# Performance work log

Hardware: AMD Instinct MI355X
Metric: run time of the kernel (lower is better)

## Reference

```python
import jax, jax.numpy as jnp
import numpy as np

NEG_INF = -1000000000.0
INPUT_SIZE = 1024
HIDDEN_SIZE = 64
B, S = 8, 2048


def setup_inputs() -> dict:
    key = jax.random.key(0)
    ks = jax.random.split(key, 8)
    scale = 1.0 / np.sqrt(INPUT_SIZE)
    inp = {
        "input": jax.random.normal(ks[0], (B, S, INPUT_SIZE), dtype=jnp.float32),
        "mask": jax.random.randint(ks[1], (B, S, S), 0, 2, dtype=jnp.int32),
        "W_q": jax.random.uniform(ks[2], (HIDDEN_SIZE, INPUT_SIZE), jnp.float32, -scale, scale),
        "b_q": jax.random.uniform(ks[3], (HIDDEN_SIZE,), jnp.float32, -scale, scale),
        "W_k": jax.random.uniform(ks[4], (HIDDEN_SIZE, INPUT_SIZE), jnp.float32, -scale, scale),
        "b_k": jax.random.uniform(ks[5], (HIDDEN_SIZE,), jnp.float32, -scale, scale),
        "W_v": jax.random.uniform(ks[6], (HIDDEN_SIZE, INPUT_SIZE), jnp.float32, -scale, scale),
        "b_v": jax.random.uniform(ks[7], (HIDDEN_SIZE,), jnp.float32, -scale, scale),
    }
    return inp


def reference(input, mask, W_q, b_q, W_k, b_k, W_v, b_v):
    inv_sqrt_d = 1.0 / np.sqrt(HIDDEN_SIZE)
    # Q/K/V projections: torch Linear is x @ W.T + b
    q = jnp.einsum('bsi,hi->bsh', input, W_q) + b_q  # (B,S,H)
    k = jnp.einsum('bsi,hi->bsh', input, W_k) + b_k
    v = jnp.einsum('bsi,hi->bsh', input, W_v) + b_v
    scores = jnp.einsum('bqh,bkh->bqk', q, k) * inv_sqrt_d  # (B,S,S)
    scores = jnp.where(mask == 0, NEG_INF, scores)
    probs = jax.nn.softmax(scores, axis=-1)
    return jnp.einsum('bqk,bkh->bqh', probs, v)  # (B,S,H)
```

## Files before the change

kernel.cpp:

```cpp
#include <hip/hip_runtime.h>

typedef __bf16 bf16;
typedef bf16 bf16x4 __attribute__((ext_vector_type(4)));
typedef bf16 bf16x8 __attribute__((ext_vector_type(8)));
typedef float floatx4 __attribute__((ext_vector_type(4)));
typedef unsigned int u32;

#define B_ 8
#define S_ 2048
#define I_ 1024
#define H_ 64

__device__ __forceinline__ void async_cp16(bf16* lds_base, const bf16* g_base, int lane) {
    __builtin_amdgcn_global_load_lds(
        (const __attribute__((address_space(1))) u32*)(g_base + lane * 8),
        (__attribute__((address_space(3))) u32*)lds_base, 16, 0, 0);
}

__global__ __launch_bounds__(256) void prep(const int* __restrict__ mask,
                                            u32* __restrict__ pm,
                                            const float* __restrict__ Wq, const float* __restrict__ bq,
                                            const float* __restrict__ Wk, const float* __restrict__ bk,
                                            const float* __restrict__ Wv, const float* __restrict__ bv,
                                            bf16* __restrict__ Wc2, float* __restrict__ bc) {
    if (blockIdx.x < 4096) {
        int d = blockIdx.x * 256 + threadIdx.x;
        const int4* src = (const int4*)(mask + (size_t)d * 32);
        u32 bits = 0;
#pragma unroll
        for (int j = 0; j < 8; ++j) {
            int4 v = src[j];
            bits |= (v.x != 0 ? 1u : 0u) << (j * 4);
            bits |= (v.y != 0 ? 1u : 0u) << (j * 4 + 1);
            bits |= (v.z != 0 ? 1u : 0u) << (j * 4 + 2);
            bits |= (v.w != 0 ? 1u : 0u) << (j * 4 + 3);
        }
        pm[d] = bits;
    } else {
        int idx = (blockIdx.x - 4096) * 256 + threadIdx.x;
        int n = idx >> 10, i = idx & 1023;
        float v;
        if (n < 64)       v = Wq[n * I_ + i] * 0.125f;
        else if (n < 128) v = Wk[(n - 64) * I_ + i];
        else              v = Wv[(n - 128) * I_ + i];
        int s = i >> 7, kl = i & 127;
        Wc2[(size_t)s * 26112 + n * 136 + kl] = (bf16)v;
        if (idx < 192) {
            float bb = (idx < 64) ? bq[idx] * 0.125f
                     : (idx < 128) ? bk[idx - 64] : bv[idx - 128];
            bc[idx] = bb;
        }
    }
}

__global__ __launch_bounds__(256, 2) void qkv_gemm(const float* __restrict__ X,
                                                   const bf16* __restrict__ Wc2,
                                                   const float* __restrict__ bc,
                                                   bf16* __restrict__ Qd,
                                                   bf16* __restrict__ Kd2,
                                                   bf16* __restrict__ Vt2) {
    __shared__ __align__(16) bf16 Xs[32 * 136];
    __shared__ __align__(16) bf16 Ws[26112];

    int tid = threadIdx.x;
    int w = tid >> 6, lane = tid & 63;
    int n = lane & 15, g = lane >> 4;
    int m0 = blockIdx.x * 32;
    int mt = w & 1, nh = (w >> 1) * 96;

    floatx4 zero4 = {0.0f, 0.0f, 0.0f, 0.0f};
    floatx4 acc[6];
#pragma unroll
    for (int t = 0; t < 6; ++t) acc[t] = zero4;

    int xrow = tid >> 3, xcb = (tid & 7) * 16;
    const float* xsrc = X + (size_t)(m0 + xrow) * I_ + xcb;
    bf16* xdst = Xs + xrow * 136 + xcb;

    float4 xr0 = *(const float4*)(xsrc);
    float4 xr1 = *(const float4*)(xsrc + 4);
    float4 xr2 = *(const float4*)(xsrc + 8);
    float4 xr3 = *(const float4*)(xsrc + 12);

    for (int s = 0; s < 8; ++s) {
#pragma unroll
        for (int i = 0; i < 13; ++i) {
            int inst = i * 4 + w;
            if (inst < 51)
                async_cp16(Ws + inst * 512, Wc2 + (size_t)s * 26112 + inst * 512, lane);
        }
        bf16x8 b0, b1;
        b0[0] = (bf16)xr0.x; b0[1] = (bf16)xr0.y; b0[2] = (bf16)xr0.z; b0[3] = (bf16)xr0.w;
        b0[4] = (bf16)xr1.x; b0[5] = (bf16)xr1.y; b0[6] = (bf16)xr1.z; b0[7] = (bf16)xr1.w;
        b1[0] = (bf16)xr2.x; b1[1] = (bf16)xr2.y; b1[2] = (bf16)xr2.z; b1[3] = (bf16)xr2.w;
        b1[4] = (bf16)xr3.x; b1[5] = (bf16)xr3.y; b1[6] = (bf16)xr3.z; b1[7] = (bf16)xr3.w;
        *(bf16x8*)xdst = b0;
        *(bf16x8*)(xdst + 8) = b1;
        __syncthreads();

        if (s < 7) {
            const float* xp = xsrc + (s + 1) * 128;
            xr0 = *(const float4*)(xp);
            xr1 = *(const float4*)(xp + 4);
            xr2 = *(const float4*)(xp + 8);
            xr3 = *(const float4*)(xp + 12);
        }

#pragma unroll
        for (int ks = 0; ks < 4; ++ks) {
            bf16x8 xa = *(bf16x8*)(Xs + (mt * 16 + n) * 136 + ks * 32 + g * 8);
#pragma unroll
            for (int nt = 0; nt < 6; ++nt) {
                bf16x8 wb = *(bf16x8*)(Ws + (nh + nt * 16 + n) * 136 + ks * 32 + g * 8);
                acc[nt] = __builtin_amdgcn_mfma_f32_16x16x32_bf16(xa, wb, acc[nt], 0, 0, 0);
            }
        }
        __syncthreads();
    }

    int b = m0 >> 11;
    int sb = (m0 & 2047) + mt * 16 + g * 4;
#pragma unroll
    for (int nt = 0; nt < 6; ++nt) {
        int ng = nh + nt * 16 + n;
        float bias = bc[ng];
        if (ng < 64) {
#pragma unroll
            for (int r = 0; r < 4; ++r)
                Qd[(size_t)(b * S_ + sb + r) * H_ + ng] = (bf16)(acc[nt][r] + bias);
        } else if (ng < 128) {
            int hc = (ng - 64) >> 3, j = (ng - 64) & 7;
#pragma unroll
            for (int r = 0; r < 4; ++r)
                Kd2[((size_t)(b * 8 + hc) * S_ + sb + r) * 8 + j] = (bf16)(acc[nt][r] + bias);
        } else {
            int hh = ng - 128, kc = sb >> 3, jj = sb & 7;
            bf16x4 pk;
#pragma unroll
            for (int r = 0; r < 4; ++r) pk[r] = (bf16)(acc[nt][r] + bias);
            *(bf16x4*)(Vt2 + ((size_t)(b * 256 + kc) * 64 + hh) * 8 + jj) = pk;
        }
    }
}

__global__ __launch_bounds__(256, 4) void attn(const bf16* __restrict__ Qd,
                                               const bf16* __restrict__ Kd2,
                                               const bf16* __restrict__ Vt2,
                                               const u32* __restrict__ pm,
                                               float* __restrict__ po,
                                               float* __restrict__ pl) {
    __shared__ __align__(16) bf16 regA[8704];
    __shared__ __align__(16) bf16 Vs[16 * 528];

    int tid = threadIdx.x;
    int w = tid >> 6, lane = tid & 63;
    int n = lane & 15, g = lane >> 4;
    int bid = blockIdx.x;
    int ksp = bid & 3;
    int qt = (bid >> 2) & 31;
    int b = bid >> 7;
    int q0 = qt * 64;

    const bf16* qptr = Qd + (size_t)(b * S_ + q0 + w * 16 + n) * H_ + g * 8;
    bf16x8 qa0 = *(const bf16x8*)qptr;
    bf16x8 qa1 = *(const bf16x8*)(qptr + 32);

    floatx4 zero4 = {0.0f, 0.0f, 0.0f, 0.0f};
    floatx4 o[4];
#pragma unroll
    for (int t = 0; t < 4; ++t) o[t] = zero4;
    float l_i[4] = {0.0f, 0.0f, 0.0f, 0.0f};

    const u32* pmb = pm + (size_t)(b * S_ + q0 + w * 16 + g * 4) * 64;

    for (int kt = ksp * 4; kt < ksp * 4 + 4; ++kt) {
        u32 mq[4][4];
#pragma unroll
        for (int r = 0; r < 4; ++r) {
            uint4 t4 = *(const uint4*)(pmb + (size_t)r * 64 + kt * 4);
            mq[r][0] = t4.x; mq[r][1] = t4.y; mq[r][2] = t4.z; mq[r][3] = t4.w;
        }
#pragma unroll
        for (int j = 0; j < 4; ++j) {
            int hc = w * 2 + (j >> 1), p = j & 1;
            async_cp16(regA + hc * 1040 + p * 512,
                       Kd2 + ((size_t)(b * 8 + hc) * S_ + kt * 128 + p * 64) * 8, lane);
        }
#pragma unroll
        for (int j = 0; j < 4; ++j) {
            int kcl = w * 4 + j;
            async_cp16(Vs + kcl * 528,
                       Vt2 + ((size_t)(b * 256 + kt * 16 + kcl) * 64) * 8, lane);
        }
        __syncthreads();

        floatx4 s[8];
#pragma unroll
        for (int nt = 0; nt < 8; ++nt) {
            floatx4 a = zero4;
            a = __builtin_amdgcn_mfma_f32_16x16x32_bf16(
                    qa0, *(const bf16x8*)(regA + g * 1040 + (nt * 16 + n) * 8), a, 0, 0, 0);
            a = __builtin_amdgcn_mfma_f32_16x16x32_bf16(
                    qa1, *(const bf16x8*)(regA + (4 + g) * 1040 + (nt * 16 + n) * 8), a, 0, 0, 0);
            s[nt] = a;
        }

#pragma unroll
        for (int r = 0; r < 4; ++r)
#pragma unroll
            for (int nt = 0; nt < 8; ++nt) {
                float e = __expf(s[nt][r]);
                bool bit = (mq[r][nt >> 1] >> ((nt & 1) * 16 + n)) & 1u;
                float p = bit ? e : 0.0f;
                s[nt][r] = p;
                l_i[r] += p;
            }
        __syncthreads();

#pragma unroll
        for (int r = 0; r < 4; ++r)
#pragma unroll
            for (int nt = 0; nt < 8; ++nt)
                regA[(w * 16 + g * 4 + r) * 136 + nt * 16 + n] = (bf16)s[nt][r];
        __syncthreads();

#pragma unroll
        for (int k0 = 0; k0 < 4; ++k0) {
            bf16x8 pa = *(bf16x8*)(regA + (w * 16 + n) * 136 + k0 * 32 + g * 8);
#pragma unroll
            for (int ht = 0; ht < 4; ++ht) {
                bf16x8 vb = *(bf16x8*)(Vs + (k0 * 4 + g) * 528 + (ht * 16 + n) * 8);
                o[ht] = __builtin_amdgcn_mfma_f32_16x16x32_bf16(pa, vb, o[ht], 0, 0, 0);
            }
        }
        __syncthreads();
    }

#pragma unroll
    for (int r = 0; r < 4; ++r)
#pragma unroll
        for (int off = 1; off < 16; off <<= 1)
            l_i[r] += __shfl_xor(l_i[r], off, 64);

    float* pb = po + (size_t)bid * 4096;
#pragma unroll
    for (int ht = 0; ht < 4; ++ht)
#pragma unroll
        for (int r = 0; r < 4; ++r)
            pb[(w * 16 + g * 4 + r) * 64 + ht * 16 + n] = o[ht][r];
    if (n == 0) {
#pragma unroll
        for (int r = 0; r < 4; ++r)
            pl[(size_t)bid * 64 + w * 16 + g * 4 + r] = l_i[r];
    }
}

__global__ __launch_bounds__(256) void reduce_o(const float* __restrict__ po,
                                                const float* __restrict__ pl,
                                                float* __restrict__ out) {
    int idx = blockIdx.x * 256 + threadIdx.x;
    int h = idx & 63, q = idx >> 6;
    int b = q >> 11, qq = q & 2047;
    int qt = qq >> 6, ql = qq & 63;
    int bid0 = (b * 32 + qt) * 4;
    float num = 0.0f, den = 0.0f;
#pragma unroll
    for (int j = 0; j < 4; ++j) {
        den += pl[(size_t)(bid0 + j) * 64 + ql];
        num += po[(size_t)(bid0 + j) * 4096 + ql * 64 + h];
    }
    out[(size_t)q * 64 + h] = num / den;
}

extern "C" void kernel_launch(void* const* d_in, const int* in_sizes, int n_in,
                              void* d_out, int out_size, void* d_ws, size_t ws_size,
                              hipStream_t stream) {
    const float* X    = (const float*)d_in[0];
    const int*   mask = (const int*)d_in[1];
    const float* Wq   = (const float*)d_in[2];
    const float* bq   = (const float*)d_in[3];
    const float* Wk   = (const float*)d_in[4];
    const float* bk   = (const float*)d_in[5];
    const float* Wv   = (const float*)d_in[6];
    const float* bv   = (const float*)d_in[7];
    float* out = (float*)d_out;

    char* p = (char*)d_ws;
    bf16* Qd   = (bf16*)p;  p += (size_t)B_ * S_ * H_ * 2;
    bf16* Kd2  = (bf16*)p;  p += (size_t)B_ * S_ * H_ * 2;
    bf16* Vt2  = (bf16*)p;  p += (size_t)B_ * S_ * H_ * 2;
    bf16* Wc2  = (bf16*)p;  p += (size_t)8 * 26112 * 2;
    float* bc  = (float*)p; p += 1024;
    u32*  pmb  = (u32*)p;   p += (size_t)B_ * S_ * 64 * 4;
    float* po  = (float*)p; p += (size_t)1024 * 4096 * 4;
    float* pl  = (float*)p; p += (size_t)1024 * 64 * 4;

    prep<<<dim3(4864), dim3(256), 0, stream>>>(mask, pmb, Wq, bq, Wk, bk, Wv, bv, Wc2, bc);
    qkv_gemm<<<dim3(512), dim3(256), 0, stream>>>(X, Wc2, bc, Qd, Kd2, Vt2);
    attn<<<dim3(1024), dim3(256), 0, stream>>>(Qd, Kd2, Vt2, pmb, po, pl);
    reduce_o<<<dim3(4096), dim3(256), 0, stream>>>(po, pl, out);
}
```

Measured before the change: 300.0 us.

## Fuse mask bit-packing into attention kernel via wave ballot

Removes the separate mask-packing pass and the packed-mask workspace. The attention kernel now reads the int32 mask directly, packs each row into bits with wave ballots into LDS, and reads the bitmask words from there. This drops one full write and read of the packed mask plus a kernel launch, but adds ballots and LDS traffic inside the attention loop. The QKV GEMM also stops prefetching the next X slice and loads it at the top of each step instead.

```diff
diff --git a/kernel.cpp b/kernel.cpp
--- a/kernel.cpp
+++ b/kernel.cpp
@@ -5,6 +5,7 @@
 typedef bf16 bf16x8 __attribute__((ext_vector_type(8)));
 typedef float floatx4 __attribute__((ext_vector_type(4)));
 typedef unsigned int u32;
+typedef unsigned long long u64;
 
 #define B_ 8
 #define S_ 2048
@@ -17,39 +18,22 @@
         (__attribute__((address_space(3))) u32*)lds_base, 16, 0, 0);
 }
 
-__global__ __launch_bounds__(256) void prep(const int* __restrict__ mask,
-                                            u32* __restrict__ pm,
-                                            const float* __restrict__ Wq, const float* __restrict__ bq,
-                                            const float* __restrict__ Wk, const float* __restrict__ bk,
-                                            const float* __restrict__ Wv, const float* __restrict__ bv,
-                                            bf16* __restrict__ Wc2, float* __restrict__ bc) {
-    if (blockIdx.x < 4096) {
-        int d = blockIdx.x * 256 + threadIdx.x;
-        const int4* src = (const int4*)(mask + (size_t)d * 32);
-        u32 bits = 0;
-#pragma unroll
-        for (int j = 0; j < 8; ++j) {
-            int4 v = src[j];
-            bits |= (v.x != 0 ? 1u : 0u) << (j * 4);
-            bits |= (v.y != 0 ? 1u : 0u) << (j * 4 + 1);
-            bits |= (v.z != 0 ? 1u : 0u) << (j * 4 + 2);
-            bits |= (v.w != 0 ? 1u : 0u) << (j * 4 + 3);
-        }
-        pm[d] = bits;
-    } else {
-        int idx = (blockIdx.x - 4096) * 256 + threadIdx.x;
-        int n = idx >> 10, i = idx & 1023;
-        float v;
-        if (n < 64)       v = Wq[n * I_ + i] * 0.125f;
-        else if (n < 128) v = Wk[(n - 64) * I_ + i];
-        else              v = Wv[(n - 128) * I_ + i];
-        int s = i >> 7, kl = i & 127;
-        Wc2[(size_t)s * 26112 + n * 136 + kl] = (bf16)v;
-        if (idx < 192) {
-            float bb = (idx < 64) ? bq[idx] * 0.125f
-                     : (idx < 128) ? bk[idx - 64] : bv[idx - 128];
-            bc[idx] = bb;
-        }
+__global__ void conv_w(const float* __restrict__ Wq, const float* __restrict__ bq,
+                       const float* __restrict__ Wk, const float* __restrict__ bk,
+                       const float* __restrict__ Wv, const float* __restrict__ bv,
+                       bf16* __restrict__ Wc2, float* __restrict__ bc) {
+    int idx = blockIdx.x * 256 + threadIdx.x;
+    int n = idx >> 10, i = idx & 1023;
+    float v;
+    if (n < 64)       v = Wq[n * I_ + i] * 0.125f;
+    else if (n < 128) v = Wk[(n - 64) * I_ + i];
+    else              v = Wv[(n - 128) * I_ + i];
+    int s = i >> 7, kl = i & 127;
+    Wc2[(size_t)s * 26112 + n * 136 + kl] = (bf16)v;
+    if (idx < 192) {
+        float bb = (idx < 64) ? bq[idx] * 0.125f
+                 : (idx < 128) ? bk[idx - 64] : bv[idx - 128];
+        bc[idx] = bb;
     }
 }
 
@@ -77,12 +61,12 @@
     const float* xsrc = X + (size_t)(m0 + xrow) * I_ + xcb;
     bf16* xdst = Xs + xrow * 136 + xcb;
 
-    float4 xr0 = *(const float4*)(xsrc);
-    float4 xr1 = *(const float4*)(xsrc + 4);
-    float4 xr2 = *(const float4*)(xsrc + 8);
-    float4 xr3 = *(const float4*)(xsrc + 12);
-
     for (int s = 0; s < 8; ++s) {
+        const float* xp = xsrc + s * 128;
+        float4 x0 = *(const float4*)(xp);
+        float4 x1 = *(const float4*)(xp + 4);
+        float4 x2 = *(const float4*)(xp + 8);
+        float4 x3 = *(const float4*)(xp + 12);
 #pragma unroll
         for (int i = 0; i < 13; ++i) {
             int inst = i * 4 + w;
@@ -90,21 +74,13 @@
                 async_cp16(Ws + inst * 512, Wc2 + (size_t)s * 26112 + inst * 512, lane);
         }
         bf16x8 b0, b1;
-        b0[0] = (bf16)xr0.x; b0[1] = (bf16)xr0.y; b0[2] = (bf16)xr0.z; b0[3] = (bf16)xr0.w;
-        b0[4] = (bf16)xr1.x; b0[5] = (bf16)xr1.y; b0[6] = (bf16)xr1.z; b0[7] = (bf16)xr1.w;
-        b1[0] = (bf16)xr2.x; b1[1] = (bf16)xr2.y; b1[2] = (bf16)xr2.z; b1[3] = (bf16)xr2.w;
-        b1[4] = (bf16)xr3.x; b1[5] = (bf16)xr3.y; b1[6] = (bf16)xr3.z; b1[7] = (bf16)xr3.w;
+        b0[0] = (bf16)x0.x; b0[1] = (bf16)x0.y; b0[2] = (bf16)x0.z; b0[3] = (bf16)x0.w;
+        b0[4] = (bf16)x1.x; b0[5] = (bf16)x1.y; b0[6] = (bf16)x1.z; b0[7] = (bf16)x1.w;
+        b1[0] = (bf16)x2.x; b1[1] = (bf16)x2.y; b1[2] = (bf16)x2.z; b1[3] = (bf16)x2.w;
+        b1[4] = (bf16)x3.x; b1[5] = (bf16)x3.y; b1[6] = (bf16)x3.z; b1[7] = (bf16)x3.w;
         *(bf16x8*)xdst = b0;
         *(bf16x8*)(xdst + 8) = b1;
         __syncthreads();
-
-        if (s < 7) {
-            const float* xp = xsrc + (s + 1) * 128;
-            xr0 = *(const float4*)(xp);
-            xr1 = *(const float4*)(xp + 4);
-            xr2 = *(const float4*)(xp + 8);
-            xr3 = *(const float4*)(xp + 12);
-        }
 
 #pragma unroll
         for (int ks = 0; ks < 4; ++ks) {
@@ -146,11 +122,12 @@
 __global__ __launch_bounds__(256, 4) void attn(const bf16* __restrict__ Qd,
                                                const bf16* __restrict__ Kd2,
                                                const bf16* __restrict__ Vt2,
-                                               const u32* __restrict__ pm,
+                                               const int* __restrict__ mask,
                                                float* __restrict__ po,
                                                float* __restrict__ pl) {
     __shared__ __align__(16) bf16 regA[8704];
     __shared__ __align__(16) bf16 Vs[16 * 528];
+    __shared__ __align__(16) u32 bfm[64][4];
 
     int tid = threadIdx.x;
     int w = tid >> 6, lane = tid & 63;
@@ -171,15 +148,15 @@
     for (int t = 0; t < 4; ++t) o[t] = zero4;
     float l_i[4] = {0.0f, 0.0f, 0.0f, 0.0f};
 
-    const u32* pmb = pm + (size_t)(b * S_ + q0 + w * 16 + g * 4) * 64;
+    const int* msl = mask + (size_t)(b * S_ + q0 + w * 16) * S_ + lane;
 
     for (int kt = ksp * 4; kt < ksp * 4 + 4; ++kt) {
-        u32 mq[4][4];
-#pragma unroll
-        for (int r = 0; r < 4; ++r) {
-            uint4 t4 = *(const uint4*)(pmb + (size_t)r * 64 + kt * 4);
-            mq[r][0] = t4.x; mq[r][1] = t4.y; mq[r][2] = t4.z; mq[r][3] = t4.w;
-        }
+        int mv[16][2];
+#pragma unroll
+        for (int rr = 0; rr < 16; ++rr)
+#pragma unroll
+            for (int c = 0; c < 2; ++c)
+                mv[rr][c] = msl[(size_t)rr * S_ + kt * 128 + c * 64];
 #pragma unroll
         for (int j = 0; j < 4; ++j) {
             int hc = w * 2 + (j >> 1), p = j & 1;
@@ -192,7 +169,24 @@
             async_cp16(Vs + kcl * 528,
                        Vt2 + ((size_t)(b * 256 + kt * 16 + kcl) * 64) * 8, lane);
         }
-        __syncthreads();
+#pragma unroll
+        for (int rr = 0; rr < 16; ++rr)
+#pragma unroll
+            for (int c = 0; c < 2; ++c) {
+                u64 bits = __ballot(mv[rr][c] != 0);
+                if (lane == 0) {
+                    bfm[w * 16 + rr][c * 2]     = (u32)bits;
+                    bfm[w * 16 + rr][c * 2 + 1] = (u32)(bits >> 32);
+                }
+            }
+        __syncthreads();
+
+        u32 mq[4][4];
+#pragma unroll
+        for (int r = 0; r < 4; ++r) {
+            uint4 t4 = *(const uint4*)&bfm[w * 16 + g * 4 + r][0];
+            mq[r][0] = t4.x; mq[r][1] = t4.y; mq[r][2] = t4.z; mq[r][3] = t4.w;
+        }
 
         floatx4 s[8];
 #pragma unroll
@@ -291,12 +285,11 @@
     bf16* Vt2  = (bf16*)p;  p += (size_t)B_ * S_ * H_ * 2;
     bf16* Wc2  = (bf16*)p;  p += (size_t)8 * 26112 * 2;
     float* bc  = (float*)p; p += 1024;
-    u32*  pmb  = (u32*)p;   p += (size_t)B_ * S_ * 64 * 4;
     float* po  = (float*)p; p += (size_t)1024 * 4096 * 4;
     float* pl  = (float*)p; p += (size_t)1024 * 64 * 4;
 
-    prep<<<dim3(4864), dim3(256), 0, stream>>>(mask, pmb, Wq, bq, Wk, bk, Wv, bv, Wc2, bc);
+    conv_w<<<dim3(768), dim3(256), 0, stream>>>(Wq, bq, Wk, bk, Wv, bv, Wc2, bc);
     qkv_gemm<<<dim3(512), dim3(256), 0, stream>>>(X, Wc2, bc, Qd, Kd2, Vt2);
-    attn<<<dim3(1024), dim3(256), 0, stream>>>(Qd, Kd2, Vt2, pmb, po, pl);
+    attn<<<dim3(1024), dim3(256), 0, stream>>>(Qd, Kd2, Vt2, mask, po, pl);
     reduce_o<<<dim3(4096), dim3(256), 0, stream>>>(po, pl, out);
 }
```

Measured after the change: 272.6 us. -9.1%, faster.
